# Kernel optimization log

Measured on AMD Instinct MI355X. Metric: run time of the kernel, lower is better.

## Reference

```python
import jax, jax.numpy as jnp
import numpy as np

B = 256          # graphs per batch
NPG = 512        # nodes per data graph
NG = B * NPG     # 131072 data-graph nodes
EG = NG * 8      # 1048576 data-graph edges
NQPG = 16        # nodes per query graph
NQ = B * NQPG    # 4096 query nodes
EQ = NQ * 8      # 32768 query edges
IN, H, L, OUT = 64, 128, 2, 1


def setup_inputs() -> dict:
    key = jax.random.key(0)
    ks = jax.random.split(key, 24)
    # edges constrained within each graph (offset + local index)
    g_off = jnp.repeat(jnp.arange(B, dtype=jnp.int32) * NPG, EG // B)
    q_off = jnp.repeat(jnp.arange(B, dtype=jnp.int32) * NQPG, EQ // B)
    inp = {
        "X": jax.random.normal(ks[0], (NG, IN), jnp.float32),
        "X_q": jax.random.normal(ks[1], (NQ, IN), jnp.float32),
        "g_src": g_off + jax.random.randint(ks[2], (EG,), 0, NPG, jnp.int32),
        "g_dst": g_off + jax.random.randint(ks[3], (EG,), 0, NPG, jnp.int32),
        "g_n2g": jnp.repeat(jnp.arange(B, dtype=jnp.int32), NPG),
        "q_src": q_off + jax.random.randint(ks[4], (EQ,), 0, NQPG, jnp.int32),
        "q_dst": q_off + jax.random.randint(ks[5], (EQ,), 0, NQPG, jnp.int32),
        "q_n2g": jnp.repeat(jnp.arange(B, dtype=jnp.int32), NQPG),
    }
    def lin(k, fi, fo):
        s = 1.0 / np.sqrt(fi)
        return jax.random.uniform(k, (fi, fo), jnp.float32, -s, s)
    inp["Wg"] = lin(ks[6], IN, H); inp["bg"] = jnp.zeros((H,), jnp.float32)
    inp["Wq"] = lin(ks[7], IN, H); inp["bq"] = jnp.zeros((H,), jnp.float32)
    inp["betas_g"] = jnp.ones((L,), jnp.float32)  # AGNN beta, init 1
    inp["betas_q"] = jnp.ones((L,), jnp.float32)
    inp["W1r"] = jnp.stack([lin(jax.random.fold_in(ks[8], l), 2 * H, H) for l in range(L)])
    inp["b1r"] = jnp.zeros((L, H), jnp.float32)
    inp["W2r"] = jnp.stack([lin(jax.random.fold_in(ks[9], l), H, H) for l in range(L)])
    inp["b2r"] = jnp.zeros((L, H), jnp.float32)
    inp["Wp1"] = lin(ks[10], H, H); inp["bp1"] = jnp.zeros((H,), jnp.float32)
    inp["Wp2"] = lin(ks[11], H, OUT); inp["bp2"] = jnp.zeros((OUT,), jnp.float32)
    return inp


def agnn(h, src, dst, beta, n):
    # DGL AGNNConv: edge logit = beta * cos(h_dst, h_src); softmax over in-edges of dst;
    # output_i = sum_j alpha_ij * h_j. Nodes with no in-edges get zeros.
    hn = h * jax.lax.rsqrt(jnp.sum(h * h, -1, keepdims=True) + 1e-24)
    e = beta * jnp.sum(hn[src] * hn[dst], -1)                      # [E]
    m = jax.ops.segment_max(e, dst, num_segments=n)
    m = jnp.where(jnp.isfinite(m), m, 0.0)
    ee = jnp.exp(e - m[dst])
    den = jax.ops.segment_sum(ee, dst, num_segments=n)             # [N]
    num = jax.ops.segment_sum(ee[:, None] * h[src], dst, num_segments=n)
    return jnp.where(den[:, None] > 0, num / jnp.maximum(den, 1e-24)[:, None], 0.0)


def reference(X, X_q, g_src, g_dst, g_n2g, q_src, q_dst, q_n2g,
              Wg, bg, Wq, bq, betas_g, betas_q, W1r, b1r, W2r, b2r,
              Wp1, bp1, Wp2, bp2):
    h_g = X @ Wg + bg              # [NG, H]
    h_q = X_q @ Wq + bq            # [NQ, H]
    for l in range(L):
        h_q = agnn(h_q, q_src, q_dst, betas_q[l], NQ)
        h_q_aggr = jax.ops.segment_sum(h_q, q_n2g, num_segments=B)        # dgl.sum_nodes -> [B, H]
        h_cat = jnp.concatenate([h_g, h_q_aggr[g_n2g]], axis=-1)          # per-node broadcast, [NG, 2H]
        h = agnn(h_cat, g_src, g_dst, betas_g[l], NG)                     # [NG, 2H]
        h_g = jax.nn.relu(h @ W1r[l] + b1r[l]) @ W2r[l] + b2r[l]          # MLP reduce -> [NG, H]
    hg_sum = jax.ops.segment_sum(h_g, g_n2g, num_segments=B)             # sum-pool per graph
    y = jax.nn.relu(hg_sum @ Wp1 + bp1) @ Wp2 + bp2                       # SumPredictor -> [B, OUT]
    return y
```

## Files before the change

kernel.cpp:

```cpp
#include <hip/hip_runtime.h>
#include <stdint.h>

#define B_   256
#define NPG  512
#define NG   131072
#define EPG  4096
#define NQPG 16
#define NQ   4096
#define EQPG 128
#define L_   2
#define HPITCH 136

typedef __attribute__((ext_vector_type(8))) short short8;
typedef __attribute__((ext_vector_type(4))) float floatx4;

__device__ inline float bf2f(unsigned short u){
    union { unsigned int i; float f; } x; x.i = ((unsigned int)u) << 16; return x.f;
}
__device__ inline unsigned short f2bf(float f){
    union { float f; unsigned int i; } x; x.f = f;
    unsigned int r = x.i + 0x7fff + ((x.i >> 16) & 1);
    return (unsigned short)(r >> 16);
}
__device__ inline float d2(unsigned int a, unsigned int b, float c){
#if __has_builtin(__builtin_amdgcn_fdot2_f32_bf16)
    typedef __attribute__((ext_vector_type(2))) __bf16 bf16x2;
    union { unsigned int u; bf16x2 v; } xa, xb;
    xa.u = a; xb.u = b;
    return __builtin_amdgcn_fdot2_f32_bf16(xa.v, xb.v, c, false);
#else
    union { unsigned int u; float f; } la, ha, lb, hb;
    la.u = a << 16; ha.u = a & 0xffff0000u;
    lb.u = b << 16; hb.u = b & 0xffff0000u;
    return fmaf(la.f, lb.f, fmaf(ha.f, hb.f, c));
#endif
}
__device__ inline float dot8(uint4 a, uint4 b){
    return d2(a.x,b.x, d2(a.y,b.y, d2(a.z,b.z, d2(a.w,b.w, 0.f))));
}
__device__ inline float dot8q(uint4 a, uint4 b, float c0){
    return d2(a.x,b.x, d2(a.y,b.y, d2(a.z,b.z, d2(a.w,b.w, c0))));
}

#if __has_builtin(__builtin_amdgcn_exp2f)
#define FEXP2(x) __builtin_amdgcn_exp2f(x)
#else
#define FEXP2(x) __expf((x) * 0.6931471805599453f)
#endif
#define LOG2E_ 1.4426950408889634f

__device__ inline float red16dpp(float v){
#if __has_builtin(__builtin_amdgcn_mov_dpp)
    int i;
    i = __builtin_amdgcn_mov_dpp(__float_as_int(v), 0xB1, 0xF, 0xF, true);
    v += __int_as_float(i);
    i = __builtin_amdgcn_mov_dpp(__float_as_int(v), 0x4E, 0xF, 0xF, true);
    v += __int_as_float(i);
    i = __builtin_amdgcn_mov_dpp(__float_as_int(v), 0x141, 0xF, 0xF, true);
    v += __int_as_float(i);
    i = __builtin_amdgcn_mov_dpp(__float_as_int(v), 0x128, 0xF, 0xF, true);
    v += __int_as_float(i);
    return v;
#else
    v += __shfl_xor(v,1); v += __shfl_xor(v,2);
    v += __shfl_xor(v,4); v += __shfl_xor(v,8);
    return v;
#endif
}

__device__ inline void red16dpp4(float& v0, float& v1, float& v2, float& v3){
#if defined(__gfx950__) || defined(__gfx942__) || defined(__gfx90a__)
    asm volatile(
        "s_nop 1\n\t"
        "v_add_f32_dpp %0, %0, %0 quad_perm:[1,0,3,2] row_mask:0xf bank_mask:0xf\n\t"
        "v_add_f32_dpp %1, %1, %1 quad_perm:[1,0,3,2] row_mask:0xf bank_mask:0xf\n\t"
        "v_add_f32_dpp %2, %2, %2 quad_perm:[1,0,3,2] row_mask:0xf bank_mask:0xf\n\t"
        "v_add_f32_dpp %3, %3, %3 quad_perm:[1,0,3,2] row_mask:0xf bank_mask:0xf\n\t"
        "v_add_f32_dpp %0, %0, %0 quad_perm:[2,3,0,1] row_mask:0xf bank_mask:0xf\n\t"
        "v_add_f32_dpp %1, %1, %1 quad_perm:[2,3,0,1] row_mask:0xf bank_mask:0xf\n\t"
        "v_add_f32_dpp %2, %2, %2 quad_perm:[2,3,0,1] row_mask:0xf bank_mask:0xf\n\t"
        "v_add_f32_dpp %3, %3, %3 quad_perm:[2,3,0,1] row_mask:0xf bank_mask:0xf\n\t"
        "v_add_f32_dpp %0, %0, %0 row_half_mirror row_mask:0xf bank_mask:0xf\n\t"
        "v_add_f32_dpp %1, %1, %1 row_half_mirror row_mask:0xf bank_mask:0xf\n\t"
        "v_add_f32_dpp %2, %2, %2 row_half_mirror row_mask:0xf bank_mask:0xf\n\t"
        "v_add_f32_dpp %3, %3, %3 row_half_mirror row_mask:0xf bank_mask:0xf\n\t"
        "v_add_f32_dpp %0, %0, %0 row_ror:8 row_mask:0xf bank_mask:0xf\n\t"
        "v_add_f32_dpp %1, %1, %1 row_ror:8 row_mask:0xf bank_mask:0xf\n\t"
        "v_add_f32_dpp %2, %2, %2 row_ror:8 row_mask:0xf bank_mask:0xf\n\t"
        "v_add_f32_dpp %3, %3, %3 row_ror:8 row_mask:0xf bank_mask:0xf"
        : "+v"(v0), "+v"(v1), "+v"(v2), "+v"(v3));
#else
    v0 = red16dpp(v0); v1 = red16dpp(v1); v2 = red16dpp(v2); v3 = red16dpp(v3);
#endif
}

#define ACCUM8(p0,p1,p2,p3,p4,p5,p6,p7,e,u) do { \
    p0 = fmaf(e, bf2f((unsigned short)((u).x&0xffffu)), p0); \
    p1 = fmaf(e, bf2f((unsigned short)((u).x>>16)),    p1); \
    p2 = fmaf(e, bf2f((unsigned short)((u).y&0xffffu)), p2); \
    p3 = fmaf(e, bf2f((unsigned short)((u).y>>16)),    p3); \
    p4 = fmaf(e, bf2f((unsigned short)((u).z&0xffffu)), p4); \
    p5 = fmaf(e, bf2f((unsigned short)((u).z>>16)),    p5); \
    p6 = fmaf(e, bf2f((unsigned short)((u).w&0xffffu)), p6); \
    p7 = fmaf(e, bf2f((unsigned short)((u).w>>16)),    p7); \
} while(0)

__global__ void k_transpose(const float* Wg, const float* Wq,
                            const float* W1r, const float* W2r,
                            unsigned short* WgT, unsigned short* WqT,
                            unsigned short* W1aT, unsigned short* W2rT){
    int idx = blockIdx.x*256 + threadIdx.x;
    if (idx < 8192){
        int k = idx >> 7, n = idx & 127; WgT[n*64 + k] = f2bf(Wg[idx]);
    } else if (idx < 16384){
        int i = idx - 8192; int k = i>>7, n = i&127; WqT[n*64+k] = f2bf(Wq[i]);
    } else if (idx < 49152){
        int i = idx - 16384; int l = i >> 14; int j = i & 16383; int k = j>>7, n = j&127;
        W1aT[l*16384 + n*128 + k] = f2bf(W1r[l*32768 + j]);
    } else {
        int i = idx - 49152; int l = i >> 14; int j = i & 16383; int k = j>>7, n = j&127;
        W2rT[l*16384 + n*128 + k] = f2bf(W2r[i]);
    }
}

__global__ __launch_bounds__(256) void k_csr(const int* __restrict__ g_src,
        const int* __restrict__ g_dst,
        unsigned short* __restrict__ csrc_g, int* __restrict__ off_g,
        float* __restrict__ degf, unsigned short* __restrict__ nodeperm){
    int g = blockIdx.x, t = threadIdx.x, lane = t & 63;
    __shared__ int cnt[NPG], woff[NPG];
    __shared__ int gscan[64];
    __shared__ int dh[64], dhoff[64];
    int gbase = g*NPG; size_t ebase = (size_t)g*EPG;
    for (int n=t;n<NPG;n+=256) cnt[n]=0;
    if (t<64) dh[t]=0;
    __syncthreads();
    for (int i=t;i<EPG;i+=256){
        int d = g_dst[ebase+i]-gbase;
        atomicAdd(&cnt[d],1);
    }
    __syncthreads();
    if (t < 64){
        int s=0;
        #pragma unroll
        for (int j=0;j<8;j++) s += cnt[t*8+j];
        int v=s;
        #pragma unroll
        for (int o=1;o<64;o<<=1){ int u=__shfl_up(v,o); if (lane>=o) v+=u; }
        gscan[t]=v;
    }
    __syncthreads();
    for (int n=t;n<NPG;n+=256){
        int grp=n>>3; int base = grp?gscan[grp-1]:0;
        for (int j=grp*8;j<n;j++) base+=cnt[j];
        off_g[g*NPG+n]=base; woff[n]=base;
        degf[gbase+n] = cnt[n]>0 ? 1.f : 0.f;
        atomicAdd(&dh[cnt[n] < 63 ? cnt[n] : 63], 1);
    }
    __syncthreads();
    if (t < 64){
        int v = dh[t];
        #pragma unroll
        for (int o=1;o<64;o<<=1){ int u=__shfl_up(v,o); if (lane>=o) v+=u; }
        dhoff[t] = v - dh[t];
    }
    __syncthreads();
    for (int n=t;n<NPG;n+=256){
        int d = cnt[n] < 63 ? cnt[n] : 63;
        int pos = atomicAdd(&dhoff[d],1);
        nodeperm[g*NPG+pos] = (unsigned short)n;
    }
    __syncthreads();
    for (int i=t;i<EPG;i+=256){
        int s = g_src[ebase+i]-gbase;
        int d = g_dst[ebase+i]-gbase;
        int pos = atomicAdd(&woff[d],1);
        csrc_g[ebase+pos]=(unsigned short)s;
    }
}

__global__ __launch_bounds__(256) void k_proj(const float* __restrict__ A,
        const unsigned short* __restrict__ Wt, const float* __restrict__ bias,
        unsigned short* __restrict__ out, float* __restrict__ nrm2){
    const int K = 64;
    int wave = threadIdx.x >> 6, lane = threadIdx.x & 63;
    int quad = lane >> 4, l16 = lane & 15;
    int wrow = blockIdx.x*64 + wave*16;
    floatx4 acc[8];
    #pragma unroll
    for (int t=0;t<8;t++){
        #pragma unroll
        for (int r=0;r<4;r++) acc[t][r]=0.f;
    }
    #pragma unroll
    for (int ks = 0; ks < 2; ks++){
        int koff = ks*32 + quad*8;
        const float* ap = A + (size_t)(wrow+l16)*K + koff;
        short8 a;
        #pragma unroll
        for (int j=0;j<8;j++) a[j] = (short)f2bf(ap[j]);
        #pragma unroll
        for (int t=0;t<8;t++){
            short8 b = *(const short8*)(Wt + (size_t)(t*16+l16)*K + koff);
            acc[t] = __builtin_amdgcn_mfma_f32_16x16x32_bf16(a, b, acc[t], 0,0,0);
        }
    }
    float ss[4] = {0.f,0.f,0.f,0.f};
    #pragma unroll
    for (int t=0;t<8;t++){
        int col = t*16 + l16;
        float bv = bias[col];
        #pragma unroll
        for (int r=0;r<4;r++){
            float v = acc[t][r] + bv;
            out[(size_t)(wrow + quad*4 + r)*128 + col] = f2bf(v);
            ss[r] += v*v;
        }
    }
    if (nrm2){
        #pragma unroll
        for (int r=0;r<4;r++){
            #pragma unroll
            for (int o=1;o<16;o<<=1) ss[r] += __shfl_xor(ss[r], o);
        }
        if (l16==0){
            #pragma unroll
            for (int r=0;r<4;r++) nrm2[wrow + quad*4 + r] = ss[r];
        }
    }
}

#define SMEM_GA 159136
__global__ __launch_bounds__(1024) void k_gagnn(const unsigned short* __restrict__ h_g,
        const float* __restrict__ nrm2, unsigned short* __restrict__ h_q,
        const int* __restrict__ q_src, const int* __restrict__ q_dst,
        const float* __restrict__ betaq_p, const float* __restrict__ betag_p,
        const unsigned short* __restrict__ csrc_g, const int* __restrict__ off_g,
        const unsigned short* __restrict__ nodeperm,
        const float* __restrict__ W1r_l, float* __restrict__ cg2,
        unsigned short* __restrict__ aout){
    extern __shared__ __align__(16) char smem[];
    unsigned short* hrows = (unsigned short*)smem;
    float* inv            = (float*)(smem + 139264);
    unsigned short* ssrc  = (unsigned short*)(smem + 141312);
    int* offc             = (int*)(smem + 149504);
    unsigned short* nprm  = (unsigned short*)(smem + 151556);
    unsigned short* hqrows= (unsigned short*)(smem + 152592);
    float* eq             = (float*)(smem + 156944);
    unsigned short* srcq  = (unsigned short*)(smem + 157456);
    unsigned short* dstq  = (unsigned short*)(smem + 157712);
    float* invq           = (float*)(smem + 157968);
    float* denq           = (float*)(smem + 158032);
    float* hqa            = (float*)(smem + 158096);
    float* cg2s           = (float*)(smem + 158608);
    float* QaccL          = (float*)(smem + 159120);
    int g = blockIdx.x, t = threadIdx.x;
    int group = t >> 4, sl = t & 15;
    float beta_q = betaq_p[0];
    float beta_g = betag_p[0];
    int gbase = g*NPG;
    size_t ebase = (size_t)g*EPG;
    for (int i=t; i<8192; i+=1024){
        int row = i >> 4, col = i & 15;
        *(uint4*)(hrows + row*HPITCH + col*8) =
            *(const uint4*)(h_g + (size_t)(gbase+row)*128 + col*8);
    }
    for (int n=t; n<NPG; n+=1024){
        inv[n] = nrm2[gbase+n];
        nprm[n] = nodeperm[g*NPG+n];
    }
    for (int i=t; i<EPG; i+=1024) ssrc[i] = csrc_g[ebase+i];
    for (int n=t; n<=NPG; n+=1024) offc[n] = (n<NPG) ? off_g[g*NPG+n] : EPG;
    if (t < 256){
        int row = t >> 4, col = t & 15;
        *(uint4*)(hqrows + row*HPITCH + col*8) =
            *(const uint4*)(h_q + (size_t)(g*NQPG+row)*128 + col*8);
    } else if (t < 384){
        int i = t - 256;
        srcq[i] = (unsigned short)(q_src[(size_t)g*EQPG+i] - g*NQPG);
        dstq[i] = (unsigned short)(q_dst[(size_t)g*EQPG+i] - g*NQPG);
    } else if (t < 400){
        denq[t-384] = 0.f;
    } else if (t == 400){
        QaccL[0] = 0.f;
    } else if (t >= 512 && t < 640){
        cg2s[t-512] = 0.f;
    }
    __syncthreads();
    if (t < 256){
        int n = t >> 4;
        uint4 u = *(const uint4*)(hqrows + n*HPITCH + sl*8);
        float s = d2(u.x,u.x, d2(u.y,u.y, d2(u.z,u.z, d2(u.w,u.w, 0.f))));
        s = red16dpp(s);
        if (sl==0) invq[n] = rsqrtf(s + 1e-24f);
    }
    __syncthreads();
    if (t < 256){
        int sg = t >> 4;
        for (int e = sg; e < EQPG; e += 16){
            int s = srcq[e], d = dstq[e];
            uint4 us = *(const uint4*)(hqrows + s*HPITCH + sl*8);
            uint4 ud = *(const uint4*)(hqrows + d*HPITCH + sl*8);
            float v = red16dpp(dot8(us, ud));
            if (sl==0){
                float ee = __expf(beta_q * v * invq[s] * invq[d]);
                eq[e] = ee;
                atomicAdd(&denq[d], ee);
            }
        }
    }
    __syncthreads();
    uint4 nq; nq.x=0; nq.y=0; nq.z=0; nq.w=0;
    int qn = t >> 4;
    if (t < 256){
        float wsum = denq[qn];
        if (wsum > 0.f){
            float a0=0,a1=0,a2=0,a3=0,a4=0,a5=0,a6=0,a7=0;
            for (int e=0;e<EQPG;e++){
                if (dstq[e] == qn){
                    float wg = eq[e];
                    int s = srcq[e];
                    uint4 u = *(const uint4*)(hqrows + s*HPITCH + sl*8);
                    ACCUM8(a0,a1,a2,a3,a4,a5,a6,a7, wg, u);
                }
            }
            float iw = __frcp_rn(wsum);
            nq.x = (unsigned int)f2bf(a0*iw) | ((unsigned int)f2bf(a1*iw)<<16);
            nq.y = (unsigned int)f2bf(a2*iw) | ((unsigned int)f2bf(a3*iw)<<16);
            nq.z = (unsigned int)f2bf(a4*iw) | ((unsigned int)f2bf(a5*iw)<<16);
            nq.w = (unsigned int)f2bf(a6*iw) | ((unsigned int)f2bf(a7*iw)<<16);
        }
    }
    __syncthreads();
    if (t < 256){
        *(uint4*)(hqrows + qn*HPITCH + sl*8) = nq;
        *(uint4*)(h_q + (size_t)(g*NQPG+qn)*128 + sl*8) = nq;
    }
    __syncthreads();
    if (t < 128){
        float s = 0.f;
        for (int n=0;n<NQPG;n++) s += bf2f(hqrows[n*HPITCH + t]);
        hqa[t] = s;
        atomicAdd(&QaccL[0], s*s);
    }
    __syncthreads();
    float Q = QaccL[0];
    for (int n=t;n<NPG;n+=1024) inv[n] = rsqrtf(inv[n] + Q + 1e-24f);
    {
        int j = t & 127, kc = t >> 7;
        float p = 0.f;
        for (int k = kc*16; k < kc*16+16; k++)
            p = fmaf(hqa[k], W1r_l[(size_t)(128+k)*128 + j], p);
        atomicAdd(&cg2s[j], p);
    }
    __syncthreads();
    if (t < 128) cg2[(size_t)g*128 + t] = cg2s[t];
    float Qs = Q * 0.0625f;
    for (int idx = group; idx < NPG; idx += 64){
        int n = nprm[idx];
        int o = offc[n];
        int c = offc[n+1] - o;
        uint4 ov;
        if (c > 0){
            uint4 ud = *(const uint4*)(hrows + n*HPITCH + sl*8);
            float bn = beta_g * inv[n] * LOG2E_;
            float ws = 0.f;
            float a0=0,a1=0,a2=0,a3=0,a4=0,a5=0,a6=0,a7=0;
            float b0=0,b1=0,b2=0,b3=0,b4=0,b5=0,b6=0,b7=0;
            int jend = o + c;
            for (int j = o; j < jend; j += 4){
                int j1 = (j+1 < jend) ? j+1 : j;
                int j2 = (j+2 < jend) ? j+2 : j;
                int j3 = (j+3 < jend) ? j+3 : j;
                int s0 = ssrc[j], s1 = ssrc[j1], s2 = ssrc[j2], s3 = ssrc[j3];
                uint4 u0 = *(const uint4*)(hrows + s0*HPITCH + sl*8);
                uint4 u1 = *(const uint4*)(hrows + s1*HPITCH + sl*8);
                uint4 u2 = *(const uint4*)(hrows + s2*HPITCH + sl*8);
                uint4 u3 = *(const uint4*)(hrows + s3*HPITCH + sl*8);
                float i0 = inv[s0], i1 = inv[s1], i2 = inv[s2], i3 = inv[s3];
                float v0 = dot8q(u0, ud, Qs);
                float v1 = dot8q(u1, ud, Qs);
                float v2 = dot8q(u2, ud, Qs);
                float v3 = dot8q(u3, ud, Qs);
                red16dpp4(v0, v1, v2, v3);
                float e0 = FEXP2(v0 * i0 * bn);
                float e1 = FEXP2(v1 * i1 * bn);
                float e2 = FEXP2(v2 * i2 * bn);
                float e3 = FEXP2(v3 * i3 * bn);
                if (j+1 >= jend) e1 = 0.f;
                if (j+2 >= jend) e2 = 0.f;
                if (j+3 >= jend) e3 = 0.f;
                ws += (e0 + e1) + (e2 + e3);
                ACCUM8(a0,a1,a2,a3,a4,a5,a6,a7, e0, u0);
                ACCUM8(b0,b1,b2,b3,b4,b5,b6,b7, e1, u1);
                ACCUM8(a0,a1,a2,a3,a4,a5,a6,a7, e2, u2);
                ACCUM8(b0,b1,b2,b3,b4,b5,b6,b7, e3, u3);
            }
            float iw = __frcp_rn(ws);
            a0+=b0; a1+=b1; a2+=b2; a3+=b3; a4+=b4; a5+=b5; a6+=b6; a7+=b7;
            ov.x = (unsigned int)f2bf(a0*iw) | ((unsigned int)f2bf(a1*iw)<<16);
            ov.y = (unsigned int)f2bf(a2*iw) | ((unsigned int)f2bf(a3*iw)<<16);
            ov.z = (unsigned int)f2bf(a4*iw) | ((unsigned int)f2bf(a5*iw)<<16);
            ov.w = (unsigned int)f2bf(a6*iw) | ((unsigned int)f2bf(a7*iw)<<16);
        } else {
            ov.x=0; ov.y=0; ov.z=0; ov.w=0;
        }
        *(uint4*)(aout + (size_t)(gbase+n)*128 + sl*8) = ov;
    }
}

#define SMEM_MLP (3*128*136*2)
__global__ __launch_bounds__(512, 2) void k_mlp_p(const unsigned short* __restrict__ A,
        const unsigned short* __restrict__ W1t, const float* __restrict__ b1,
        const float* __restrict__ cg2, const float* __restrict__ degf,
        const unsigned short* __restrict__ W2t, const float* __restrict__ b2,
        unsigned short* __restrict__ out, float* __restrict__ nrm2){
    extern __shared__ __align__(16) char smem[];
    unsigned short* W1s = (unsigned short*)smem;
    unsigned short* W2s = W1s + 128*136;
    unsigned short* h1  = W2s + 128*136;
    int t = threadIdx.x;
    int g = blockIdx.x;
    #pragma unroll
    for (int p=0;p<4;p++){
        int flat = p*4096 + t*8;
        int n = flat>>7, k = flat&127;
        *(uint4*)(W1s + n*136 + k) = *(const uint4*)(W1t + n*128 + k);
        *(uint4*)(W2s + n*136 + k) = *(const uint4*)(W2t + n*128 + k);
    }
    __syncthreads();
    int wave = t>>6, lane = t&63, quad = lane>>4, l16 = lane&15;
    const float* cg = cg2 + (size_t)g*128;
    short8 af[4];
    {
        int wrow = g*512 + wave*16;
        #pragma unroll
        for (int ks=0;ks<4;ks++)
            af[ks] = *(const short8*)(A + (size_t)(wrow+l16)*128 + ks*32 + quad*8);
    }
    for (int it=0; it<4; it++){
        int wrow = g*512 + it*128 + wave*16;
        floatx4 acc[8];
        #pragma unroll
        for (int t8=0;t8<8;t8++){
            #pragma unroll
            for (int r=0;r<4;r++) acc[t8][r]=0.f;
        }
        #pragma unroll
        for (int ks=0;ks<4;ks++){
            int koff = ks*32 + quad*8;
            #pragma unroll
            for (int t8=0;t8<8;t8++){
                short8 b = *(const short8*)(W1s + (t8*16+l16)*136 + koff);
                acc[t8] = __builtin_amdgcn_mfma_f32_16x16x32_bf16(af[ks], b, acc[t8], 0,0,0);
            }
        }
        float dg[4];
        #pragma unroll
        for (int r=0;r<4;r++) dg[r] = degf[wrow + quad*4 + r];
        #pragma unroll
        for (int t8=0;t8<8;t8++){
            int col = t8*16 + l16;
            float bv = b1[col];
            float cv = cg[col];
            #pragma unroll
            for (int r=0;r<4;r++){
                float v = acc[t8][r] + bv + dg[r]*cv;
                v = v > 0.f ? v : 0.f;
                h1[(wave*16 + quad*4 + r)*136 + col] = f2bf(v);
            }
        }
        __syncthreads();
        short8 afn[4];
        if (it < 3){
            int wrow_n = g*512 + (it+1)*128 + wave*16;
            #pragma unroll
            for (int ks=0;ks<4;ks++)
                afn[ks] = *(const short8*)(A + (size_t)(wrow_n+l16)*128 + ks*32 + quad*8);
        }
        short8 hf[4];
        #pragma unroll
        for (int ks=0;ks<4;ks++) hf[ks] = *(const short8*)(h1 + (wave*16+l16)*136 + ks*32 + quad*8);
        floatx4 acc2[8];
        #pragma unroll
        for (int t8=0;t8<8;t8++){
            #pragma unroll
            for (int r=0;r<4;r++) acc2[t8][r]=0.f;
        }
        #pragma unroll
        for (int ks=0;ks<4;ks++){
            int koff = ks*32 + quad*8;
            #pragma unroll
            for (int t8=0;t8<8;t8++){
                short8 b = *(const short8*)(W2s + (t8*16+l16)*136 + koff);
                acc2[t8] = __builtin_amdgcn_mfma_f32_16x16x32_bf16(hf[ks], b, acc2[t8], 0,0,0);
            }
        }
        float ss[4] = {0.f,0.f,0.f,0.f};
        #pragma unroll
        for (int t8=0;t8<8;t8++){
            int col = t8*16 + l16;
            float bv = b2[col];
            #pragma unroll
            for (int r=0;r<4;r++){
                float v = acc2[t8][r] + bv;
                out[(size_t)(wrow + quad*4 + r)*128 + col] = f2bf(v);
                ss[r] += v*v;
            }
        }
        #pragma unroll
        for (int r=0;r<4;r++){
            #pragma unroll
            for (int o=1;o<16;o<<=1) ss[r] += __shfl_xor(ss[r], o);
        }
        if (l16==0){
            #pragma unroll
            for (int r=0;r<4;r++) nrm2[wrow + quad*4 + r] = ss[r];
        }
        __syncthreads();
        #pragma unroll
        for (int ks=0;ks<4;ks++) af[ks] = afn[ks];
    }
}

__global__ __launch_bounds__(512) void k_hgpred(const unsigned short* __restrict__ h_g,
        const float* __restrict__ Wp1, const float* __restrict__ bp1,
        const float* __restrict__ Wp2, const float* __restrict__ bp2,
        float* __restrict__ y){
    __shared__ float red[32][128];
    __shared__ float hsum[128];
    __shared__ float red2[128];
    int g = blockIdx.x, t = threadIdx.x;
    int c = t & 15, r0 = t >> 4;
    float s[8];
    #pragma unroll
    for (int k=0;k<8;k++) s[k]=0.f;
    for (int i=0;i<16;i++){
        int row = r0 + i*32;
        uint4 u = *(const uint4*)(h_g + (size_t)(g*NPG + row)*128 + c*8);
        s[0] += bf2f((unsigned short)(u.x&0xffff)); s[1] += bf2f((unsigned short)(u.x>>16));
        s[2] += bf2f((unsigned short)(u.y&0xffff)); s[3] += bf2f((unsigned short)(u.y>>16));
        s[4] += bf2f((unsigned short)(u.z&0xffff)); s[5] += bf2f((unsigned short)(u.z>>16));
        s[6] += bf2f((unsigned short)(u.w&0xffff)); s[7] += bf2f((unsigned short)(u.w>>16));
    }
    #pragma unroll
    for (int k=0;k<8;k++) red[r0][c*8+k] = s[k];
    __syncthreads();
    if (t < 128){
        float a = 0.f;
        #pragma unroll
        for (int r=0;r<32;r++) a += red[r][t];
        hsum[t] = a;
    }
    __syncthreads();
    if (t < 128){
        float acc = bp1[t];
        for (int k=0;k<128;k++) acc += hsum[k]*Wp1[k*128+t];
        acc = fmaxf(acc, 0.f);
        red2[t] = acc * Wp2[t];
    }
    __syncthreads();
    for (int s2=64; s2>0; s2>>=1){
        if (t<s2) red2[t]+=red2[t+s2];
        __syncthreads();
    }
    if (t==0) y[g] = red2[0] + bp2[0];
}

extern "C" void kernel_launch(void* const* d_in, const int* in_sizes, int n_in,
                              void* d_out, int out_size, void* d_ws, size_t ws_size,
                              hipStream_t stream) {
    const float* X    = (const float*)d_in[0];
    const float* X_q  = (const float*)d_in[1];
    const int* g_src = (const int*)d_in[2];
    const int* g_dst = (const int*)d_in[3];
    const int* q_src = (const int*)d_in[5];
    const int* q_dst = (const int*)d_in[6];
    const float* Wg   = (const float*)d_in[8];
    const float* bg   = (const float*)d_in[9];
    const float* Wq   = (const float*)d_in[10];
    const float* bq   = (const float*)d_in[11];
    const float* betas_g = (const float*)d_in[12];
    const float* betas_q = (const float*)d_in[13];
    const float* W1r  = (const float*)d_in[14];
    const float* b1r  = (const float*)d_in[15];
    const float* W2r  = (const float*)d_in[16];
    const float* b2r  = (const float*)d_in[17];
    const float* Wp1  = (const float*)d_in[18];
    const float* bp1  = (const float*)d_in[19];
    const float* Wp2  = (const float*)d_in[20];
    const float* bp2  = (const float*)d_in[21];

    uint8_t* w = (uint8_t*)d_ws;
    unsigned short* h_g  = (unsigned short*)w;    w += (size_t)NG*128*2;
    unsigned short* h_q  = (unsigned short*)w;    w += (size_t)NQ*128*2;
    unsigned short* aout = (unsigned short*)w;    w += (size_t)NG*128*2;
    float* nrm2  = (float*)w;                     w += (size_t)NG*4;
    float* degf  = (float*)w;                     w += (size_t)NG*4;
    float* cg2   = (float*)w;                     w += (size_t)B_*128*4;
    unsigned short* WgT   = (unsigned short*)w;   w += 8192*2;
    unsigned short* WqT   = (unsigned short*)w;   w += 8192*2;
    unsigned short* W1aT  = (unsigned short*)w;   w += 2*16384*2;
    unsigned short* W2rT  = (unsigned short*)w;   w += 2*16384*2;
    unsigned short* csrc_g = (unsigned short*)w;  w += (size_t)B_*EPG*2;
    unsigned short* nodeperm = (unsigned short*)w; w += (size_t)B_*NPG*2;
    int* off_g = (int*)w;                         w += (size_t)B_*NPG*4;

    static bool attr_done = false;
    if (!attr_done){
        hipFuncSetAttribute((const void*)k_mlp_p,
                            hipFuncAttributeMaxDynamicSharedMemorySize, SMEM_MLP);
        hipFuncSetAttribute((const void*)k_gagnn,
                            hipFuncAttributeMaxDynamicSharedMemorySize, SMEM_GA);
        attr_done = true;
    }

    k_transpose<<<320,256,0,stream>>>(Wg,Wq,W1r,W2r,WgT,WqT,W1aT,W2rT);
    k_csr<<<B_,256,0,stream>>>(g_src,g_dst,csrc_g,off_g,degf,nodeperm);
    k_proj<<<NG/64,256,0,stream>>>(X,   WgT, bg, h_g, nrm2);
    k_proj<<<NQ/64,256,0,stream>>>(X_q, WqT, bq, h_q, nullptr);
    for (int l=0;l<L_;l++){
        k_gagnn<<<B_,1024,SMEM_GA,stream>>>(h_g, nrm2, h_q, q_src, q_dst,
                                            betas_q + l, betas_g + l,
                                            csrc_g, off_g, nodeperm,
                                            W1r + l*32768, cg2, aout);
        k_mlp_p<<<B_,512,SMEM_MLP,stream>>>(aout, W1aT + l*16384, b1r + l*128, cg2, degf,
                                            W2rT + l*16384, b2r + l*128, h_g, nrm2);
    }
    k_hgpred<<<B_,512,0,stream>>>(h_g, Wp1, bp1, Wp2, bp2, (float*)d_out);
}
```

Before: 301.6 us.

## Split query AGNN into one kernel and spread graph edge aggregation across blocks

All query-graph AGNN layers now run in one small up-front kernel that stores per-graph Q values and cg2 vectors for both layers. The per-graph edge aggregation used to run as one 1024-thread block per graph with the whole graph staged in LDS. It now runs as 8 blocks per graph that read node rows straight from global memory or L2. The inverse norms, with Q folded in, are computed in the projection and MLP epilogues, which removes the rsqrt pass and the LDS staging. The aim is more blocks in flight and no large shared-memory footprint, at the cost of scattered global gathers and the loss of the dual accumulators.

```diff
diff --git a/kernel.cpp b/kernel.cpp
--- a/kernel.cpp
+++ b/kernel.cpp
@@ -181,7 +181,8 @@
 
 __global__ __launch_bounds__(256) void k_proj(const float* __restrict__ A,
         const unsigned short* __restrict__ Wt, const float* __restrict__ bias,
-        unsigned short* __restrict__ out, float* __restrict__ nrm2){
+        unsigned short* __restrict__ out, float* __restrict__ invout,
+        const float* __restrict__ Qv0){
     const int K = 64;
     int wave = threadIdx.x >> 6, lane = threadIdx.x & 63;
     int quad = lane >> 4, l16 = lane & 15;
@@ -217,7 +218,7 @@
             ss[r] += v*v;
         }
     }
-    if (nrm2){
+    if (invout){
         #pragma unroll
         for (int r=0;r<4;r++){
             #pragma unroll
@@ -225,79 +226,49 @@
         }
         if (l16==0){
             #pragma unroll
-            for (int r=0;r<4;r++) nrm2[wrow + quad*4 + r] = ss[r];
-        }
-    }
-}
-
-#define SMEM_GA 159136
-__global__ __launch_bounds__(1024) void k_gagnn(const unsigned short* __restrict__ h_g,
-        const float* __restrict__ nrm2, unsigned short* __restrict__ h_q,
+            for (int r=0;r<4;r++){
+                int row = wrow + quad*4 + r;
+                invout[row] = rsqrtf(ss[r] + Qv0[row>>9] + 1e-24f);
+            }
+        }
+    }
+}
+
+__global__ __launch_bounds__(256) void k_queryall(
+        const unsigned short* __restrict__ h_q,
         const int* __restrict__ q_src, const int* __restrict__ q_dst,
-        const float* __restrict__ betaq_p, const float* __restrict__ betag_p,
-        const unsigned short* __restrict__ csrc_g, const int* __restrict__ off_g,
-        const unsigned short* __restrict__ nodeperm,
-        const float* __restrict__ W1r_l, float* __restrict__ cg2,
-        unsigned short* __restrict__ aout){
-    extern __shared__ __align__(16) char smem[];
-    unsigned short* hrows = (unsigned short*)smem;
-    float* inv            = (float*)(smem + 139264);
-    unsigned short* ssrc  = (unsigned short*)(smem + 141312);
-    int* offc             = (int*)(smem + 149504);
-    unsigned short* nprm  = (unsigned short*)(smem + 151556);
-    unsigned short* hqrows= (unsigned short*)(smem + 152592);
-    float* eq             = (float*)(smem + 156944);
-    unsigned short* srcq  = (unsigned short*)(smem + 157456);
-    unsigned short* dstq  = (unsigned short*)(smem + 157712);
-    float* invq           = (float*)(smem + 157968);
-    float* denq           = (float*)(smem + 158032);
-    float* hqa            = (float*)(smem + 158096);
-    float* cg2s           = (float*)(smem + 158608);
-    float* QaccL          = (float*)(smem + 159120);
-    int g = blockIdx.x, t = threadIdx.x;
-    int group = t >> 4, sl = t & 15;
-    float beta_q = betaq_p[0];
-    float beta_g = betag_p[0];
-    int gbase = g*NPG;
-    size_t ebase = (size_t)g*EPG;
-    for (int i=t; i<8192; i+=1024){
-        int row = i >> 4, col = i & 15;
-        *(uint4*)(hrows + row*HPITCH + col*8) =
-            *(const uint4*)(h_g + (size_t)(gbase+row)*128 + col*8);
-    }
-    for (int n=t; n<NPG; n+=1024){
-        inv[n] = nrm2[gbase+n];
-        nprm[n] = nodeperm[g*NPG+n];
-    }
-    for (int i=t; i<EPG; i+=1024) ssrc[i] = csrc_g[ebase+i];
-    for (int n=t; n<=NPG; n+=1024) offc[n] = (n<NPG) ? off_g[g*NPG+n] : EPG;
-    if (t < 256){
-        int row = t >> 4, col = t & 15;
-        *(uint4*)(hqrows + row*HPITCH + col*8) =
-            *(const uint4*)(h_q + (size_t)(g*NQPG+row)*128 + col*8);
-    } else if (t < 384){
-        int i = t - 256;
-        srcq[i] = (unsigned short)(q_src[(size_t)g*EQPG+i] - g*NQPG);
-        dstq[i] = (unsigned short)(q_dst[(size_t)g*EQPG+i] - g*NQPG);
-    } else if (t < 400){
-        denq[t-384] = 0.f;
-    } else if (t == 400){
-        QaccL[0] = 0.f;
-    } else if (t >= 512 && t < 640){
-        cg2s[t-512] = 0.f;
-    }
-    __syncthreads();
-    if (t < 256){
-        int n = t >> 4;
-        uint4 u = *(const uint4*)(hqrows + n*HPITCH + sl*8);
-        float s = d2(u.x,u.x, d2(u.y,u.y, d2(u.z,u.z, d2(u.w,u.w, 0.f))));
-        s = red16dpp(s);
-        if (sl==0) invq[n] = rsqrtf(s + 1e-24f);
-    }
-    __syncthreads();
-    if (t < 256){
-        int sg = t >> 4;
-        for (int e = sg; e < EQPG; e += 16){
+        const float* __restrict__ betas_q,
+        const float* __restrict__ W1r,
+        float* __restrict__ Qv, float* __restrict__ cg2a){
+    __shared__ unsigned short hqrows[NQPG*HPITCH];
+    __shared__ float eq[EQPG];
+    __shared__ unsigned short srcq[EQPG], dstq[EQPG];
+    __shared__ float invq[NQPG], denq[NQPG], hqa[128], cg2s[128];
+    __shared__ float QaccL;
+    int g = blockIdx.x, t = threadIdx.x, sl = t & 15;
+    {
+        int row = t >> 4;
+        *(uint4*)(hqrows + row*HPITCH + sl*8) =
+            *(const uint4*)(h_q + (size_t)(g*NQPG+row)*128 + sl*8);
+    }
+    if (t < EQPG){
+        srcq[t] = (unsigned short)(q_src[(size_t)g*EQPG+t] - g*NQPG);
+        dstq[t] = (unsigned short)(q_dst[(size_t)g*EQPG+t] - g*NQPG);
+    }
+    int qn = t >> 4;
+    for (int l=0; l<L_; l++){
+        float beta_q = betas_q[l];
+        if (t < NQPG) denq[t] = 0.f;
+        if (t == 16) QaccL = 0.f;
+        if (t >= 128 && t < 256) cg2s[t-128] = 0.f;
+        __syncthreads();
+        {
+            uint4 u = *(const uint4*)(hqrows + qn*HPITCH + sl*8);
+            float s = red16dpp(dot8(u,u));
+            if (sl==0) invq[qn] = rsqrtf(s + 1e-24f);
+        }
+        __syncthreads();
+        for (int e = qn; e < EQPG; e += 16){
             int s = srcq[e], d = dstq[e];
             uint4 us = *(const uint4*)(hqrows + s*HPITCH + sl*8);
             uint4 ud = *(const uint4*)(hqrows + d*HPITCH + sl*8);
@@ -308,76 +279,98 @@
                 atomicAdd(&denq[d], ee);
             }
         }
-    }
-    __syncthreads();
-    uint4 nq; nq.x=0; nq.y=0; nq.z=0; nq.w=0;
-    int qn = t >> 4;
-    if (t < 256){
-        float wsum = denq[qn];
-        if (wsum > 0.f){
-            float a0=0,a1=0,a2=0,a3=0,a4=0,a5=0,a6=0,a7=0;
-            for (int e=0;e<EQPG;e++){
-                if (dstq[e] == qn){
-                    float wg = eq[e];
-                    int s = srcq[e];
-                    uint4 u = *(const uint4*)(hqrows + s*HPITCH + sl*8);
-                    ACCUM8(a0,a1,a2,a3,a4,a5,a6,a7, wg, u);
+        __syncthreads();
+        uint4 nq; nq.x=0; nq.y=0; nq.z=0; nq.w=0;
+        {
+            float wsum = denq[qn];
+            if (wsum > 0.f){
+                float a0=0,a1=0,a2=0,a3=0,a4=0,a5=0,a6=0,a7=0;
+                for (int e=0;e<EQPG;e++){
+                    if (dstq[e] == qn){
+                        float wg = eq[e];
+                        int s = srcq[e];
+                        uint4 u = *(const uint4*)(hqrows + s*HPITCH + sl*8);
+                        ACCUM8(a0,a1,a2,a3,a4,a5,a6,a7, wg, u);
+                    }
                 }
-            }
-            float iw = __frcp_rn(wsum);
-            nq.x = (unsigned int)f2bf(a0*iw) | ((unsigned int)f2bf(a1*iw)<<16);
-            nq.y = (unsigned int)f2bf(a2*iw) | ((unsigned int)f2bf(a3*iw)<<16);
-            nq.z = (unsigned int)f2bf(a4*iw) | ((unsigned int)f2bf(a5*iw)<<16);
-            nq.w = (unsigned int)f2bf(a6*iw) | ((unsigned int)f2bf(a7*iw)<<16);
-        }
-    }
-    __syncthreads();
-    if (t < 256){
+                float iw = __frcp_rn(wsum);
+                nq.x = (unsigned int)f2bf(a0*iw) | ((unsigned int)f2bf(a1*iw)<<16);
+                nq.y = (unsigned int)f2bf(a2*iw) | ((unsigned int)f2bf(a3*iw)<<16);
+                nq.z = (unsigned int)f2bf(a4*iw) | ((unsigned int)f2bf(a5*iw)<<16);
+                nq.w = (unsigned int)f2bf(a6*iw) | ((unsigned int)f2bf(a7*iw)<<16);
+            }
+        }
+        __syncthreads();
         *(uint4*)(hqrows + qn*HPITCH + sl*8) = nq;
-        *(uint4*)(h_q + (size_t)(g*NQPG+qn)*128 + sl*8) = nq;
-    }
-    __syncthreads();
-    if (t < 128){
-        float s = 0.f;
-        for (int n=0;n<NQPG;n++) s += bf2f(hqrows[n*HPITCH + t]);
-        hqa[t] = s;
-        atomicAdd(&QaccL[0], s*s);
-    }
-    __syncthreads();
-    float Q = QaccL[0];
-    for (int n=t;n<NPG;n+=1024) inv[n] = rsqrtf(inv[n] + Q + 1e-24f);
-    {
-        int j = t & 127, kc = t >> 7;
-        float p = 0.f;
-        for (int k = kc*16; k < kc*16+16; k++)
-            p = fmaf(hqa[k], W1r_l[(size_t)(128+k)*128 + j], p);
-        atomicAdd(&cg2s[j], p);
-    }
-    __syncthreads();
-    if (t < 128) cg2[(size_t)g*128 + t] = cg2s[t];
+        __syncthreads();
+        if (t < 128){
+            float s = 0.f;
+            for (int n=0;n<NQPG;n++) s += bf2f(hqrows[n*HPITCH + t]);
+            hqa[t] = s;
+            atomicAdd(&QaccL, s*s);
+        }
+        __syncthreads();
+        if (t == 0) Qv[l*B_+g] = QaccL;
+        {
+            int jj = t & 127, kc = t >> 7;
+            const float* Wl = W1r + (size_t)l*32768;
+            float p = 0.f;
+            for (int k = kc*64; k < kc*64+64; k++)
+                p = fmaf(hqa[k], Wl[(size_t)(128+k)*128 + jj], p);
+            atomicAdd(&cg2s[jj], p);
+        }
+        __syncthreads();
+        if (t < 128) cg2a[((size_t)l*B_+g)*128 + t] = cg2s[t];
+        __syncthreads();
+    }
+}
+
+__global__ __launch_bounds__(256, 8) void k_gedge(
+        const unsigned short* __restrict__ h_g,
+        const float* __restrict__ invg,
+        const float* __restrict__ betag_p,
+        const float* __restrict__ Qv_l,
+        const unsigned short* __restrict__ csrc_g,
+        const int* __restrict__ off_g,
+        const unsigned short* __restrict__ nodeperm,
+        unsigned short* __restrict__ aout){
+    int bid = blockIdx.x;
+    int g = (((bid >> 3) & 31) << 3) | (bid & 7);
+    int jblk = bid >> 8;
+    int t = threadIdx.x, sg = t >> 4, sl = t & 15;
+    int gbase = g*NPG;
+    float beta_g = betag_p[0];
+    float Q = Qv_l[g];
     float Qs = Q * 0.0625f;
-    for (int idx = group; idx < NPG; idx += 64){
-        int n = nprm[idx];
-        int o = offc[n];
-        int c = offc[n+1] - o;
+    const uint4* hb4 = (const uint4*)(h_g + (size_t)gbase*128) + sl;
+    uint4* ab4 = (uint4*)(aout + (size_t)gbase*128) + sl;
+    const float* invb = invg + gbase;
+    const unsigned short* csb = csrc_g + (size_t)g*EPG;
+    const int* ofb = off_g + g*NPG;
+    const unsigned short* npb = nodeperm + g*NPG;
+    #pragma unroll
+    for (int k=0;k<4;k++){
+        int idx = ((sg*4 + k) << 3) | jblk;
+        int n = npb[idx];
+        int o = ofb[n];
+        int c = ((n < NPG-1) ? ofb[n+1] : EPG) - o;
         uint4 ov;
         if (c > 0){
-            uint4 ud = *(const uint4*)(hrows + n*HPITCH + sl*8);
-            float bn = beta_g * inv[n] * LOG2E_;
+            uint4 ud = hb4[n*16];
+            float bn = beta_g * invb[n] * LOG2E_;
             float ws = 0.f;
             float a0=0,a1=0,a2=0,a3=0,a4=0,a5=0,a6=0,a7=0;
-            float b0=0,b1=0,b2=0,b3=0,b4=0,b5=0,b6=0,b7=0;
             int jend = o + c;
             for (int j = o; j < jend; j += 4){
                 int j1 = (j+1 < jend) ? j+1 : j;
                 int j2 = (j+2 < jend) ? j+2 : j;
                 int j3 = (j+3 < jend) ? j+3 : j;
-                int s0 = ssrc[j], s1 = ssrc[j1], s2 = ssrc[j2], s3 = ssrc[j3];
-                uint4 u0 = *(const uint4*)(hrows + s0*HPITCH + sl*8);
-                uint4 u1 = *(const uint4*)(hrows + s1*HPITCH + sl*8);
-                uint4 u2 = *(const uint4*)(hrows + s2*HPITCH + sl*8);
-                uint4 u3 = *(const uint4*)(hrows + s3*HPITCH + sl*8);
-                float i0 = inv[s0], i1 = inv[s1], i2 = inv[s2], i3 = inv[s3];
+                int s0 = csb[j], s1 = csb[j1], s2 = csb[j2], s3 = csb[j3];
+                uint4 u0 = hb4[s0*16];
+                uint4 u1 = hb4[s1*16];
+                uint4 u2 = hb4[s2*16];
+                uint4 u3 = hb4[s3*16];
+                float i0 = invb[s0], i1 = invb[s1], i2 = invb[s2], i3 = invb[s3];
                 float v0 = dot8q(u0, ud, Qs);
                 float v1 = dot8q(u1, ud, Qs);
                 float v2 = dot8q(u2, ud, Qs);
@@ -392,12 +385,11 @@
                 if (j+3 >= jend) e3 = 0.f;
                 ws += (e0 + e1) + (e2 + e3);
                 ACCUM8(a0,a1,a2,a3,a4,a5,a6,a7, e0, u0);
-                ACCUM8(b0,b1,b2,b3,b4,b5,b6,b7, e1, u1);
+                ACCUM8(a0,a1,a2,a3,a4,a5,a6,a7, e1, u1);
                 ACCUM8(a0,a1,a2,a3,a4,a5,a6,a7, e2, u2);
-                ACCUM8(b0,b1,b2,b3,b4,b5,b6,b7, e3, u3);
+                ACCUM8(a0,a1,a2,a3,a4,a5,a6,a7, e3, u3);
             }
             float iw = __frcp_rn(ws);
-            a0+=b0; a1+=b1; a2+=b2; a3+=b3; a4+=b4; a5+=b5; a6+=b6; a7+=b7;
             ov.x = (unsigned int)f2bf(a0*iw) | ((unsigned int)f2bf(a1*iw)<<16);
             ov.y = (unsigned int)f2bf(a2*iw) | ((unsigned int)f2bf(a3*iw)<<16);
             ov.z = (unsigned int)f2bf(a4*iw) | ((unsigned int)f2bf(a5*iw)<<16);
@@ -405,7 +397,7 @@
         } else {
             ov.x=0; ov.y=0; ov.z=0; ov.w=0;
         }
-        *(uint4*)(aout + (size_t)(gbase+n)*128 + sl*8) = ov;
+        ab4[n*16] = ov;
     }
 }
 
@@ -414,13 +406,15 @@
         const unsigned short* __restrict__ W1t, const float* __restrict__ b1,
         const float* __restrict__ cg2, const float* __restrict__ degf,
         const unsigned short* __restrict__ W2t, const float* __restrict__ b2,
-        unsigned short* __restrict__ out, float* __restrict__ nrm2){
+        unsigned short* __restrict__ out, float* __restrict__ invout,
+        const float* __restrict__ Qnext){
     extern __shared__ __align__(16) char smem[];
     unsigned short* W1s = (unsigned short*)smem;
     unsigned short* W2s = W1s + 128*136;
     unsigned short* h1  = W2s + 128*136;
     int t = threadIdx.x;
     int g = blockIdx.x;
+    float Qn = Qnext ? Qnext[g] : 0.f;
     #pragma unroll
     for (int p=0;p<4;p++){
         int flat = p*4096 + t*8;
@@ -508,14 +502,19 @@
                 ss[r] += v*v;
             }
         }
-        #pragma unroll
-        for (int r=0;r<4;r++){
-            #pragma unroll
-            for (int o=1;o<16;o<<=1) ss[r] += __shfl_xor(ss[r], o);
-        }
-        if (l16==0){
-            #pragma unroll
-            for (int r=0;r<4;r++) nrm2[wrow + quad*4 + r] = ss[r];
+        if (Qnext){
+            #pragma unroll
+            for (int r=0;r<4;r++){
+                #pragma unroll
+                for (int o=1;o<16;o<<=1) ss[r] += __shfl_xor(ss[r], o);
+            }
+            if (l16==0){
+                #pragma unroll
+                for (int r=0;r<4;r++){
+                    int row = wrow + quad*4 + r;
+                    invout[row] = rsqrtf(ss[r] + Qn + 1e-24f);
+                }
+            }
         }
         __syncthreads();
         #pragma unroll
@@ -595,9 +594,10 @@
     unsigned short* h_g  = (unsigned short*)w;    w += (size_t)NG*128*2;
     unsigned short* h_q  = (unsigned short*)w;    w += (size_t)NQ*128*2;
     unsigned short* aout = (unsigned short*)w;    w += (size_t)NG*128*2;
-    float* nrm2  = (float*)w;                     w += (size_t)NG*4;
+    float* invg  = (float*)w;                     w += (size_t)NG*4;
     float* degf  = (float*)w;                     w += (size_t)NG*4;
-    float* cg2   = (float*)w;                     w += (size_t)B_*128*4;
+    float* Qv    = (float*)w;                     w += (size_t)L_*B_*4;
+    float* cg2a  = (float*)w;                     w += (size_t)L_*B_*128*4;
     unsigned short* WgT   = (unsigned short*)w;   w += 8192*2;
     unsigned short* WqT   = (unsigned short*)w;   w += 8192*2;
     unsigned short* W1aT  = (unsigned short*)w;   w += 2*16384*2;
@@ -610,22 +610,22 @@
     if (!attr_done){
         hipFuncSetAttribute((const void*)k_mlp_p,
                             hipFuncAttributeMaxDynamicSharedMemorySize, SMEM_MLP);
-        hipFuncSetAttribute((const void*)k_gagnn,
-                            hipFuncAttributeMaxDynamicSharedMemorySize, SMEM_GA);
         attr_done = true;
     }
 
     k_transpose<<<320,256,0,stream>>>(Wg,Wq,W1r,W2r,WgT,WqT,W1aT,W2rT);
     k_csr<<<B_,256,0,stream>>>(g_src,g_dst,csrc_g,off_g,degf,nodeperm);
-    k_proj<<<NG/64,256,0,stream>>>(X,   WgT, bg, h_g, nrm2);
-    k_proj<<<NQ/64,256,0,stream>>>(X_q, WqT, bq, h_q, nullptr);
+    k_proj<<<NQ/64,256,0,stream>>>(X_q, WqT, bq, h_q, nullptr, nullptr);
+    k_queryall<<<B_,256,0,stream>>>(h_q, q_src, q_dst, betas_q, W1r, Qv, cg2a);
+    k_proj<<<NG/64,256,0,stream>>>(X, WgT, bg, h_g, invg, Qv);
     for (int l=0;l<L_;l++){
-        k_gagnn<<<B_,1024,SMEM_GA,stream>>>(h_g, nrm2, h_q, q_src, q_dst,
-                                            betas_q + l, betas_g + l,
-                                            csrc_g, off_g, nodeperm,
-                                            W1r + l*32768, cg2, aout);
-        k_mlp_p<<<B_,512,SMEM_MLP,stream>>>(aout, W1aT + l*16384, b1r + l*128, cg2, degf,
-                                            W2rT + l*16384, b2r + l*128, h_g, nrm2);
+        k_gedge<<<B_*8,256,0,stream>>>(h_g, invg, betas_g + l, Qv + l*B_,
+                                       csrc_g, off_g, nodeperm, aout);
+        k_mlp_p<<<B_,512,SMEM_MLP,stream>>>(aout, W1aT + l*16384, b1r + l*128,
+                                            cg2a + (size_t)l*B_*128, degf,
+                                            W2rT + l*16384, b2r + l*128, h_g,
+                                            (l==0) ? invg : nullptr,
+                                            (l==0) ? (Qv + B_) : nullptr);
     }
     k_hgpred<<<B_,512,0,stream>>>(h_g, Wp1, bp1, Wp2, bp2, (float*)d_out);
 }
```

New measurement: 370.9 us. 1.23x slower.
